# Kernel optimization log

Measured on AMD Instinct MI355X. Metric: run time of the kernel, lower is better.

Reference implementation:

```python
import jax, jax.numpy as jnp
import numpy as np

B, T, I, H = 512, 256, 256, 512


def setup_inputs() -> dict:
    key = jax.random.key(0)
    k1, k2, k3, k4, k5 = jax.random.split(key, 5)
    s = 1.0 / np.sqrt(H)  # torch LSTMCell init scale
    return {
        "x": jax.random.normal(k1, (B, T, I), dtype=jnp.float32),
        "W_ih": jax.random.uniform(k2, (4 * H, I), dtype=jnp.float32, minval=-s, maxval=s),
        "W_hh": jax.random.uniform(k3, (4 * H, H), dtype=jnp.float32, minval=-s, maxval=s),
        "b_ih": jax.random.uniform(k4, (4 * H,), dtype=jnp.float32, minval=-s, maxval=s),
        "b_hh": jax.random.uniform(k5, (4 * H,), dtype=jnp.float32, minval=-s, maxval=s),
    }


def _att_lstm(x, W_ih, W_hh, b_ih, b_hh):
    batch, hidden = x.shape[0], W_hh.shape[1]
    b = b_ih + b_hh  # (4H,)

    def step(carry, xt):
        h, c = carry
        gates = xt @ W_ih.T + h @ W_hh.T + b  # (B, 4H)
        i, f, g, o = jnp.split(gates, 4, axis=-1)  # torch gate order: i, f, g, o
        i = jax.nn.sigmoid(i)
        f = jax.nn.sigmoid(f)
        g = jnp.tanh(g)
        o = jax.nn.sigmoid(o)
        c_new = f * c + i * g
        h_new = o * jnp.tanh(c_new)
        return (h_new, c_new), h_new

    h0 = jnp.zeros((batch, hidden), dtype=x.dtype)
    c0 = jnp.zeros((batch, hidden), dtype=x.dtype)
    (h_last, _), h_seq = jax.lax.scan(step, (h0, c0), jnp.swapaxes(x, 0, 1))
    h_states = jnp.swapaxes(h_seq, 0, 1)  # (B, T, H)

    # attention pooling: plain score normalization (NOT softmax), as in source
    att_score = jnp.einsum("bth,bh->bt", h_states, h_last)  # (B, T)
    att_dist = att_score / jnp.sum(att_score, axis=1, keepdims=True)
    context = jnp.einsum("bt,bth->bh", att_dist, h_states)  # (B, H)
    return context[:, None, :]  # (B, 1, H)


def reference(x, W_ih, W_hh, b_ih, b_hh):
    return _att_lstm(x, W_ih, W_hh, b_ih, b_hh)
```

## Files before the change

### kernel.cpp

```cpp
#include <hip/hip_runtime.h>

#define BATCH 512
#define TT    256
#define II    256
#define HH    512

typedef float f32x4  __attribute__((ext_vector_type(4)));
typedef unsigned short u16x8 __attribute__((ext_vector_type(8)));
typedef short bfrag  __attribute__((ext_vector_type(8)));

__device__ inline unsigned short f2bf(float f) {
    unsigned u = __float_as_uint(f);
    return (unsigned short)((u + 0x7fffu + ((u >> 16) & 1u)) >> 16);
}
__device__ inline float bf2f(unsigned short h) { return __uint_as_float(((unsigned)h) << 16); }

__device__ inline bfrag cvt8(const float* p) {
    float4 a = *(const float4*)p;
    float4 b = *(const float4*)(p + 4);
    u16x8 u;
    u[0]=f2bf(a.x); u[1]=f2bf(a.y); u[2]=f2bf(a.z); u[3]=f2bf(a.w);
    u[4]=f2bf(b.x); u[5]=f2bf(b.y); u[6]=f2bf(b.z); u[7]=f2bf(b.w);
    return __builtin_bit_cast(bfrag, u);
}
__device__ inline bfrag ld8(const unsigned short* p) {
    return __builtin_bit_cast(bfrag, *(const u16x8*)p);
}
__device__ inline float sigm(float x) { return 1.f / (1.f + __expf(-x)); }
__device__ inline float tanh_(float x) {
    float ax = fabsf(x);
    float e  = __expf(-2.f * ax);
    float t  = (1.f - e) / (1.f + e);
    return copysignf(t, x);
}

__global__ __launch_bounds__(256) void cast_x_kernel(const float* __restrict__ x,
                                                     unsigned short* __restrict__ xt) {
    int b  = blockIdx.x >> 2;
    int t0 = (blockIdx.x & 3) * 64;
    int ic = (threadIdx.x & 31) * 8;
    int tq = threadIdx.x >> 5;
#pragma unroll
    for (int p = 0; p < 8; ++p) {
        int t = t0 + tq * 8 + p;
        const float* src = x + ((long)b * TT + t) * II + ic;
        float4 a = *(const float4*)src;
        float4 bb = *(const float4*)(src + 4);
        u16x8 u;
        u[0]=f2bf(a.x); u[1]=f2bf(a.y); u[2]=f2bf(a.z); u[3]=f2bf(a.w);
        u[4]=f2bf(bb.x); u[5]=f2bf(bb.y); u[6]=f2bf(bb.z); u[7]=f2bf(bb.w);
        *(u16x8*)(xt + ((long)t * BATCH + b) * II + ic) = u;
    }
}

__global__ __launch_bounds__(256, 1) void lstm_persist(
    const float* __restrict__ Wih, const float* __restrict__ Whh,
    const float* __restrict__ bih, const float* __restrict__ bhh,
    const unsigned short* __restrict__ xb,
    unsigned short* __restrict__ hs,
    unsigned int* __restrict__ flags)
{
    const int tid  = threadIdx.x;
    const int bx   = blockIdx.x;
    const int grp  = bx >> 4;
    const int wg   = bx & 15;
    const int w    = tid >> 6;
    const int lane = tid & 63;
    const int quad = lane >> 4;
    const int ct   = lane & 15;
    const bool lo  = (ct < 8);
    const int rb0  = grp * 32;
    const int hcol = wg * 32 + w * 8 + (ct & 7);

    __shared__ unsigned short sh[32 * 520];
    __shared__ unsigned short wlds[128 * 264];

    int wrow[2];
    wrow[0] = ((ct >> 3) + 0) * HH + hcol;
    wrow[1] = ((ct >> 3) + 2) * HH + hcol;

    bfrag wih_f[8][2], whh_r[8][2];
#pragma unroll
    for (int kk = 0; kk < 8; ++kk)
#pragma unroll
        for (int nt = 0; nt < 2; ++nt) {
            wih_f[kk][nt] = cvt8(Wih + (long)wrow[nt] * II + kk * 32 + quad * 8);
            whh_r[kk][nt] = cvt8(Whh + (long)wrow[nt] * HH + kk * 32 + quad * 8);
        }

    for (int e = tid * 8; e < 128 * 256; e += 256 * 8) {
        int lc = e >> 8;
        int k  = e & 255;
        int row = (lc >> 5) * HH + wg * 32 + (lc & 31);
        bfrag f = cvt8(Whh + (long)row * HH + 256 + k);
        *(u16x8*)(wlds + lc * 264 + k) = __builtin_bit_cast(u16x8, f);
    }
    __syncthreads();

    const int wl0 = ((((ct >> 3) + 0) * 32 + w * 8 + (ct & 7)) * 264) + quad * 8;
    const int wl1 = ((((ct >> 3) + 2) * 32 + w * 8 + (ct & 7)) * 264) + quad * 8;

    float bb[2];
    bb[0] = bih[wrow[0]] + bhh[wrow[0]];
    bb[1] = bih[wrow[1]] + bhh[wrow[1]];

    float cst[2][4];
#pragma unroll
    for (int mt = 0; mt < 2; ++mt)
#pragma unroll
        for (int r = 0; r < 4; ++r) cst[mt][r] = 0.f;

    for (int t = 0; t < TT; ++t) {
        f32x4 acc[2][2];
#pragma unroll
        for (int mt = 0; mt < 2; ++mt)
#pragma unroll
            for (int nt = 0; nt < 2; ++nt)
                acc[mt][nt] = (f32x4){bb[nt], bb[nt], bb[nt], bb[nt]};

#pragma unroll
        for (int kk = 0; kk < 8; ++kk) {
#pragma unroll
            for (int mt = 0; mt < 2; ++mt) {
                bfrag a = ld8(xb + ((long)t * BATCH + rb0 + mt * 16 + ct) * II + kk * 32 + quad * 8);
#pragma unroll
                for (int nt = 0; nt < 2; ++nt)
                    acc[mt][nt] = __builtin_amdgcn_mfma_f32_16x16x32_bf16(a, wih_f[kk][nt], acc[mt][nt], 0, 0, 0);
            }
        }

        if (t > 0) {
            if (w == 0) {
                const unsigned* fp = flags + (((grp * TT + (t - 1)) << 4) | (lane & 15));
                unsigned v;
                do {
                    asm volatile("global_load_dword %0, %1, off sc0 sc1\n\ts_waitcnt vmcnt(0)"
                                 : "=v"(v) : "v"(fp) : "memory");
                } while (!__all(v != 0u));
            }
            __syncthreads();

            uint4 vv[8];
#pragma unroll
            for (int j = 0; j < 8; ++j) {
                int cid = j * 256 + tid;
                int row = cid >> 6, c16 = cid & 63;
                const unsigned short* p = hs + ((long)(rb0 + row) * TT + (t - 1)) * HH + c16 * 8;
                asm volatile("global_load_dwordx4 %0, %1, off sc0 sc1"
                             : "=v"(vv[j]) : "v"(p));
            }
            asm volatile("s_waitcnt vmcnt(0)" ::: "memory");
#pragma unroll
            for (int j = 0; j < 8; ++j) {
                int cid = j * 256 + tid;
                int row = cid >> 6, c16 = cid & 63;
                *(uint4*)(sh + row * 520 + c16 * 8) = vv[j];
            }
            __syncthreads();

#pragma unroll
            for (int kk = 0; kk < 8; ++kk) {
                bfrag a[2];
#pragma unroll
                for (int mt = 0; mt < 2; ++mt)
                    a[mt] = ld8(sh + (mt * 16 + ct) * 520 + kk * 32 + quad * 8);
#pragma unroll
                for (int mt = 0; mt < 2; ++mt)
#pragma unroll
                    for (int nt = 0; nt < 2; ++nt)
                        acc[mt][nt] = __builtin_amdgcn_mfma_f32_16x16x32_bf16(a[mt], whh_r[kk][nt], acc[mt][nt], 0, 0, 0);
            }
#pragma unroll
            for (int kk = 0; kk < 8; ++kk) {
                bfrag a[2], b[2];
#pragma unroll
                for (int mt = 0; mt < 2; ++mt)
                    a[mt] = ld8(sh + (mt * 16 + ct) * 520 + (8 + kk) * 32 + quad * 8);
                b[0] = ld8(wlds + wl0 + kk * 32);
                b[1] = ld8(wlds + wl1 + kk * 32);
#pragma unroll
                for (int mt = 0; mt < 2; ++mt)
#pragma unroll
                    for (int nt = 0; nt < 2; ++nt)
                        acc[mt][nt] = __builtin_amdgcn_mfma_f32_16x16x32_bf16(a[mt], b[nt], acc[mt][nt], 0, 0, 0);
            }
        }

#pragma unroll
        for (int mt = 0; mt < 2; ++mt) {
#pragma unroll
            for (int r = 0; r < 4; ++r) {
                float a0 = acc[mt][0][r], a1 = acc[mt][1][r];
                float b0 = __shfl_xor(a0, 8, 64);
                float b1 = __shfl_xor(a1, 8, 64);
                float iv = lo ? a0 : b0;
                float fv = lo ? b0 : a0;
                float gv = lo ? a1 : b1;
                float ov = lo ? b1 : a1;
                iv = sigm(iv); fv = sigm(fv); gv = tanh_(gv); ov = sigm(ov);
                float c = fv * cst[mt][r] + iv * gv;
                cst[mt][r] = c;
                float h = ov * tanh_(c);
                if (lo) {
                    int b = rb0 + mt * 16 + quad * 4 + r;
                    unsigned short* p = hs + ((long)b * TT + t) * HH + hcol;
                    unsigned hv = f2bf(h);
                    asm volatile("global_store_short %0, %1, off sc0 sc1"
                                 :: "v"(p), "v"(hv) : "memory");
                }
            }
        }

        asm volatile("s_waitcnt vmcnt(0)" ::: "memory");
        __syncthreads();
        if (tid == 0 && t < TT - 1) {
            unsigned one = 1u;
            unsigned* p = flags + (((grp * TT + t) << 4) | wg);
            asm volatile("global_store_dword %0, %1, off sc0 sc1"
                         :: "v"(p), "v"(one) : "memory");
        }
    }
}

__global__ __launch_bounds__(256) void attn_kernel(const unsigned short* __restrict__ hs,
                                                   float* __restrict__ out) {
    int b = blockIdx.x, tid = threadIdx.x;
    int w = tid >> 6, lane = tid & 63;
    __shared__ float sc[TT];
    __shared__ float hl[HH];
    for (int c = tid; c < HH; c += 256)
        hl[c] = bf2f(hs[((long)b * TT + (TT - 1)) * HH + c]);
    __syncthreads();
    float hr[8];
#pragma unroll
    for (int j = 0; j < 8; ++j) hr[j] = hl[lane * 8 + j];
    for (int t = w; t < TT; t += 4) {
        u16x8 hv = *(const u16x8*)(hs + ((long)b * TT + t) * HH + lane * 8);
        float p = 0.f;
#pragma unroll
        for (int j = 0; j < 8; ++j) p += bf2f(hv[j]) * hr[j];
#pragma unroll
        for (int off = 32; off; off >>= 1) p += __shfl_xor(p, off, 64);
        if (lane == 0) sc[t] = p;
    }
    __syncthreads();
    float denom = 0.f;
    for (int t = 0; t < TT; ++t) denom += sc[t];
    float c0 = 0.f, c1 = 0.f;
    int col = tid * 2;
    for (int t = 0; t < TT; ++t) {
        float s = sc[t];
        unsigned v = *(const unsigned*)(hs + ((long)b * TT + t) * HH + col);
        c0 += s * __uint_as_float((v & 0xffffu) << 16);
        c1 += s * __uint_as_float(v & 0xffff0000u);
    }
    out[(long)b * HH + col]     = c0 / denom;
    out[(long)b * HH + col + 1] = c1 / denom;
}

extern "C" void kernel_launch(void* const* d_in, const int* in_sizes, int n_in,
                              void* d_out, int out_size, void* d_ws, size_t ws_size,
                              hipStream_t stream) {
    const float* x   = (const float*)d_in[0];
    const float* Wih = (const float*)d_in[1];
    const float* Whh = (const float*)d_in[2];
    const float* bih = (const float*)d_in[3];
    const float* bhh = (const float*)d_in[4];
    float* out = (float*)d_out;

    char* ws = (char*)d_ws;
    unsigned int*   flags = (unsigned int*)ws;
    unsigned short* hs    = (unsigned short*)(ws + 262144);
    unsigned short* xb    = (unsigned short*)(ws + 262144 + (size_t)BATCH * TT * HH * 2);

    (void)hipMemsetAsync(flags, 0, 262144, stream);
    cast_x_kernel<<<BATCH * (TT / 64), 256, 0, stream>>>(x, xb);
    lstm_persist<<<256, 256, 0, stream>>>(Wih, Whh, bih, bhh, xb, hs, flags);
    attn_kernel<<<BATCH, 256, 0, stream>>>(hs, out);
}
```

Before: 1.974 ms.

## Overlap next-step input GEMM with sync and exchange h via compact ring

```diff
diff --git a/kernel.cpp b/kernel.cpp
--- a/kernel.cpp
+++ b/kernel.cpp
@@ -6,6 +6,7 @@
 #define HH    512
 
 typedef float f32x4  __attribute__((ext_vector_type(4)));
+typedef unsigned u32x4 __attribute__((ext_vector_type(4)));
 typedef unsigned short u16x8 __attribute__((ext_vector_type(8)));
 typedef short bfrag  __attribute__((ext_vector_type(8)));
 
@@ -58,7 +59,8 @@
     const float* __restrict__ bih, const float* __restrict__ bhh,
     const unsigned short* __restrict__ xb,
     unsigned short* __restrict__ hs,
-    unsigned int* __restrict__ flags)
+    unsigned short* __restrict__ ring,
+    unsigned char* __restrict__ flags)
 {
     const int tid  = threadIdx.x;
     const int bx   = blockIdx.x;
@@ -72,8 +74,9 @@
     const int rb0  = grp * 32;
     const int hcol = wg * 32 + w * 8 + (ct & 7);
 
-    __shared__ unsigned short sh[32 * 520];
-    __shared__ unsigned short wlds[128 * 264];
+    __shared__ unsigned short sh[32 * 528];
+    __shared__ unsigned short wlds[128 * 272];
+    __shared__ unsigned short sh2[32 * 32];
 
     int wrow[2];
     wrow[0] = ((ct >> 3) + 0) * HH + hcol;
@@ -93,12 +96,12 @@
         int k  = e & 255;
         int row = (lc >> 5) * HH + wg * 32 + (lc & 31);
         bfrag f = cvt8(Whh + (long)row * HH + 256 + k);
-        *(u16x8*)(wlds + lc * 264 + k) = __builtin_bit_cast(u16x8, f);
+        *(u16x8*)(wlds + lc * 272 + k) = __builtin_bit_cast(u16x8, f);
     }
     __syncthreads();
 
-    const int wl0 = ((((ct >> 3) + 0) * 32 + w * 8 + (ct & 7)) * 264) + quad * 8;
-    const int wl1 = ((((ct >> 3) + 2) * 32 + w * 8 + (ct & 7)) * 264) + quad * 8;
+    const int wl0 = ((((ct >> 3) + 0) * 32 + w * 8 + (ct & 7)) * 272) + quad * 8;
+    const int wl1 = ((((ct >> 3) + 2) * 32 + w * 8 + (ct & 7)) * 272) + quad * 8;
 
     float bb[2];
     bb[0] = bih[wrow[0]] + bhh[wrow[0]];
@@ -110,42 +113,42 @@
 #pragma unroll
         for (int r = 0; r < 4; ++r) cst[mt][r] = 0.f;
 
+    f32x4 acc[2][2];
+#pragma unroll
+    for (int mt = 0; mt < 2; ++mt)
+#pragma unroll
+        for (int nt = 0; nt < 2; ++nt)
+            acc[mt][nt] = (f32x4){bb[nt], bb[nt], bb[nt], bb[nt]};
+#pragma unroll
+    for (int kk = 0; kk < 8; ++kk)
+#pragma unroll
+        for (int mt = 0; mt < 2; ++mt) {
+            bfrag a = ld8(xb + ((long)0 * BATCH + rb0 + mt * 16 + ct) * II + kk * 32 + quad * 8);
+#pragma unroll
+            for (int nt = 0; nt < 2; ++nt)
+                acc[mt][nt] = __builtin_amdgcn_mfma_f32_16x16x32_bf16(a, wih_f[kk][nt], acc[mt][nt], 0, 0, 0);
+        }
+
     for (int t = 0; t < TT; ++t) {
-        f32x4 acc[2][2];
-#pragma unroll
-        for (int mt = 0; mt < 2; ++mt)
-#pragma unroll
-            for (int nt = 0; nt < 2; ++nt)
-                acc[mt][nt] = (f32x4){bb[nt], bb[nt], bb[nt], bb[nt]};
-
-#pragma unroll
-        for (int kk = 0; kk < 8; ++kk) {
-#pragma unroll
-            for (int mt = 0; mt < 2; ++mt) {
-                bfrag a = ld8(xb + ((long)t * BATCH + rb0 + mt * 16 + ct) * II + kk * 32 + quad * 8);
-#pragma unroll
-                for (int nt = 0; nt < 2; ++nt)
-                    acc[mt][nt] = __builtin_amdgcn_mfma_f32_16x16x32_bf16(a, wih_f[kk][nt], acc[mt][nt], 0, 0, 0);
-            }
-        }
-
         if (t > 0) {
-            if (w == 0) {
-                const unsigned* fp = flags + (((grp * TT + (t - 1)) << 4) | (lane & 15));
-                unsigned v;
+            if (tid == 0) {
+                const unsigned char* fp = flags + (((long)grp * TT + (t - 1)) << 4);
+                u32x4 fv;
                 do {
-                    asm volatile("global_load_dword %0, %1, off sc0 sc1\n\ts_waitcnt vmcnt(0)"
-                                 : "=v"(v) : "v"(fp) : "memory");
-                } while (!__all(v != 0u));
+                    asm volatile("global_load_dwordx4 %0, %1, off sc0 sc1\n\ts_waitcnt vmcnt(0)"
+                                 : "=v"(fv) : "v"(fp) : "memory");
+                } while (fv.x != 0x01010101u || fv.y != 0x01010101u ||
+                         fv.z != 0x01010101u || fv.w != 0x01010101u);
             }
             __syncthreads();
 
-            uint4 vv[8];
+            const unsigned short* rbase = ring + (((long)grp * 4 + ((t - 1) & 3)) * 32) * HH;
+            u32x4 vv[8];
 #pragma unroll
             for (int j = 0; j < 8; ++j) {
                 int cid = j * 256 + tid;
                 int row = cid >> 6, c16 = cid & 63;
-                const unsigned short* p = hs + ((long)(rb0 + row) * TT + (t - 1)) * HH + c16 * 8;
+                const unsigned short* p = rbase + row * HH + c16 * 8;
                 asm volatile("global_load_dwordx4 %0, %1, off sc0 sc1"
                              : "=v"(vv[j]) : "v"(p));
             }
@@ -154,7 +157,7 @@
             for (int j = 0; j < 8; ++j) {
                 int cid = j * 256 + tid;
                 int row = cid >> 6, c16 = cid & 63;
-                *(uint4*)(sh + row * 520 + c16 * 8) = vv[j];
+                *(u32x4*)(sh + row * 528 + c16 * 8) = vv[j];
             }
             __syncthreads();
 
@@ -163,7 +166,7 @@
                 bfrag a[2];
 #pragma unroll
                 for (int mt = 0; mt < 2; ++mt)
-                    a[mt] = ld8(sh + (mt * 16 + ct) * 520 + kk * 32 + quad * 8);
+                    a[mt] = ld8(sh + (mt * 16 + ct) * 528 + kk * 32 + quad * 8);
 #pragma unroll
                 for (int mt = 0; mt < 2; ++mt)
 #pragma unroll
@@ -175,7 +178,7 @@
                 bfrag a[2], b[2];
 #pragma unroll
                 for (int mt = 0; mt < 2; ++mt)
-                    a[mt] = ld8(sh + (mt * 16 + ct) * 520 + (8 + kk) * 32 + quad * 8);
+                    a[mt] = ld8(sh + (mt * 16 + ct) * 528 + (8 + kk) * 32 + quad * 8);
                 b[0] = ld8(wlds + wl0 + kk * 32);
                 b[1] = ld8(wlds + wl1 + kk * 32);
 #pragma unroll
@@ -201,23 +204,45 @@
                 float c = fv * cst[mt][r] + iv * gv;
                 cst[mt][r] = c;
                 float h = ov * tanh_(c);
-                if (lo) {
-                    int b = rb0 + mt * 16 + quad * 4 + r;
-                    unsigned short* p = hs + ((long)b * TT + t) * HH + hcol;
-                    unsigned hv = f2bf(h);
-                    asm volatile("global_store_short %0, %1, off sc0 sc1"
-                                 :: "v"(p), "v"(hv) : "memory");
+                if (lo)
+                    sh2[(mt * 16 + quad * 4 + r) * 32 + w * 8 + (ct & 7)] = f2bf(h);
+            }
+        }
+        __syncthreads();
+
+        if (tid < 128) {
+            int row = tid >> 2, c = tid & 3;
+            u32x4 v = *(const u32x4*)(sh2 + row * 32 + c * 8);
+            *(u32x4*)(hs + ((long)(rb0 + row) * TT + t) * HH + wg * 32 + c * 8) = v;
+            unsigned short* rp = ring + (((long)grp * 4 + (t & 3)) * 32 + row) * HH + wg * 32 + c * 8;
+            asm volatile("global_store_dwordx4 %0, %1, off sc0 sc1"
+                         :: "v"(rp), "v"(v) : "memory");
+        }
+
+        if (t < TT - 1) {
+#pragma unroll
+            for (int mt = 0; mt < 2; ++mt)
+#pragma unroll
+                for (int nt = 0; nt < 2; ++nt)
+                    acc[mt][nt] = (f32x4){bb[nt], bb[nt], bb[nt], bb[nt]};
+#pragma unroll
+            for (int kk = 0; kk < 8; ++kk)
+#pragma unroll
+                for (int mt = 0; mt < 2; ++mt) {
+                    bfrag a = ld8(xb + ((long)(t + 1) * BATCH + rb0 + mt * 16 + ct) * II + kk * 32 + quad * 8);
+#pragma unroll
+                    for (int nt = 0; nt < 2; ++nt)
+                        acc[mt][nt] = __builtin_amdgcn_mfma_f32_16x16x32_bf16(a, wih_f[kk][nt], acc[mt][nt], 0, 0, 0);
                 }
-            }
-        }
-
-        asm volatile("s_waitcnt vmcnt(0)" ::: "memory");
-        __syncthreads();
-        if (tid == 0 && t < TT - 1) {
-            unsigned one = 1u;
-            unsigned* p = flags + (((grp * TT + t) << 4) | wg);
-            asm volatile("global_store_dword %0, %1, off sc0 sc1"
-                         :: "v"(p), "v"(one) : "memory");
+
+            asm volatile("s_waitcnt vmcnt(0)" ::: "memory");
+            __syncthreads();
+            if (tid == 0) {
+                unsigned one = 1u;
+                unsigned char* p = flags + ((((long)grp * TT + t) << 4) | wg);
+                asm volatile("global_store_byte %0, %1, off sc0 sc1"
+                             :: "v"(p), "v"(one) : "memory");
+            }
         }
     }
 }
@@ -269,12 +294,13 @@
     float* out = (float*)d_out;
 
     char* ws = (char*)d_ws;
-    unsigned int*   flags = (unsigned int*)ws;
-    unsigned short* hs    = (unsigned short*)(ws + 262144);
-    unsigned short* xb    = (unsigned short*)(ws + 262144 + (size_t)BATCH * TT * HH * 2);
-
-    (void)hipMemsetAsync(flags, 0, 262144, stream);
+    unsigned char*  flags = (unsigned char*)ws;
+    unsigned short* ring  = (unsigned short*)(ws + 65536);
+    unsigned short* hs    = (unsigned short*)(ws + 65536 + 2097152);
+    unsigned short* xb    = (unsigned short*)(ws + 65536 + 2097152 + (size_t)BATCH * TT * HH * 2);
+
+    (void)hipMemsetAsync(flags, 0, 65536, stream);
     cast_x_kernel<<<BATCH * (TT / 64), 256, 0, stream>>>(x, xb);
-    lstm_persist<<<256, 256, 0, stream>>>(Wih, Whh, bih, bhh, xb, hs, flags);
+    lstm_persist<<<256, 256, 0, stream>>>(Wih, Whh, bih, bhh, xb, hs, ring, flags);
     attn_kernel<<<BATCH, 256, 0, stream>>>(hs, out);
 }
```

New measurement: 2.010 ms. No clear change (+1.8%).
